# Kernel optimization log

Hardware: AMD Instinct MI355X
Metric: run time of the kernel (lower is better)

## Reference

```python
import jax, jax.numpy as jnp
import numpy as np

NEG_SLOPE = 0.2  # PyG GATConv default


def gat_conv(h, src, dst, n_nodes, W, a_src, a_dst, bias, concat):
    """PyG-style GATConv (single linear shared across src/dst, self-loops
    already included in src/dst). W: [heads*out, in]; a_*: [heads, out]."""
    heads, out = a_src.shape
    g = (h @ W.T).reshape(-1, heads, out)  # [N, H, D]
    # per-node attention logits, then gather scalars per edge (PyG order)
    al_src = jnp.einsum('nhd,hd->nh', g, a_src)  # [N, H]
    al_dst = jnp.einsum('nhd,hd->nh', g, a_dst)
    e = jax.nn.leaky_relu(al_src[src] + al_dst[dst], NEG_SLOPE)  # [E, H]
    # segment softmax over incoming edges of each dst node
    e_max = jax.ops.segment_max(e, dst, num_segments=n_nodes)
    e_exp = jnp.exp(e - e_max[dst])
    denom = jax.ops.segment_sum(e_exp, dst, num_segments=n_nodes)
    alpha = e_exp / denom[dst]  # every node has a self-loop -> denom > 0
    msg = g[src] * alpha[..., None]  # [E, H, D]
    out_n = jax.ops.segment_sum(msg, dst, num_segments=n_nodes)  # [N, H, D]
    if concat:
        out_n = out_n.reshape(n_nodes, heads * out)
    else:
        out_n = out_n.mean(axis=1)
    return out_n + bias


def setup_inputs() -> dict:
    key = jax.random.key(0)
    ks = jax.random.split(key, 20)
    N, M = 100000, 1600000
    node_dim, edge_dim, global_dim = 12, 5, 11
    hidden, heads, num_targets = 32, 4, 4
    in1 = node_dim + global_dim  # 23
    s = 0.1
    inp = {
        'x': jax.random.normal(ks[0], (N, node_dim), jnp.float32),
        'edge_index': jax.random.randint(ks[1], (2, M), 0, N, jnp.int32),
        'edge_attr': jax.random.normal(ks[2], (M, edge_dim), jnp.float32),
        'u': jax.random.normal(ks[3], (1, global_dim), jnp.float32),
        # conv1: in1 -> hidden per head, concat
        'W1': jax.random.normal(ks[4], (heads * hidden, in1), jnp.float32) * s,
        'a_src1': jax.random.normal(ks[5], (heads, hidden), jnp.float32) * s,
        'a_dst1': jax.random.normal(ks[6], (heads, hidden), jnp.float32) * s,
        'b1': jnp.zeros((heads * hidden,), jnp.float32),
        # conv2: heads*hidden -> hidden, mean over heads
        'W2': jax.random.normal(ks[7], (heads * hidden, heads * hidden), jnp.float32) * s,
        'a_src2': jax.random.normal(ks[8], (heads, hidden), jnp.float32) * s,
        'a_dst2': jax.random.normal(ks[9], (heads, hidden), jnp.float32) * s,
        'b2': jnp.zeros((hidden,), jnp.float32),
        # decoder: (2*hidden + edge_dim) -> 2*hidden -> hidden -> num_targets
        'dw1': jax.random.normal(ks[10], (2 * hidden, 2 * hidden + edge_dim), jnp.float32) * s,
        'db1': jnp.zeros((2 * hidden,), jnp.float32),
        'dw2': jax.random.normal(ks[11], (hidden, 2 * hidden), jnp.float32) * s,
        'db2': jnp.zeros((hidden,), jnp.float32),
        'dw3': jax.random.normal(ks[12], (num_targets, hidden), jnp.float32) * s,
        'db3': jnp.zeros((num_targets,), jnp.float32),
    }
    return inp


def reference(x, edge_index, edge_attr, u, W1, a_src1, a_dst1, b1,
              W2, a_src2, a_dst2, b2, dw1, db1, dw2, db2, dw3, db3):
    N = x.shape[0]
    loop = jnp.arange(N, dtype=edge_index.dtype)
    src = jnp.concatenate([edge_index[0], loop])  # add self-loops (PyG default)
    dst = jnp.concatenate([edge_index[1], loop])

    u_node = jnp.broadcast_to(u, (N, u.shape[-1]))
    h = jnp.concatenate([x, u_node], axis=-1)  # [N, 23]

    h = jax.nn.elu(gat_conv(h, src, dst, N, W1, a_src1, a_dst1, b1, True))
    h = jax.nn.elu(gat_conv(h, src, dst, N, W2, a_src2, a_dst2, b2, False))

    s0, d0 = edge_index[0], edge_index[1]
    e_in = jnp.concatenate([h[s0], h[d0], edge_attr], axis=-1)  # [M, 69]
    z = jax.nn.relu(e_in @ dw1.T + db1)
    z = jax.nn.relu(z @ dw2.T + db2)
    return z @ dw3.T + db3  # [M, num_targets]
```

## Files before the change

### kernel.cpp

```cpp
#include <hip/hip_runtime.h>

#define DEVINL __device__ __forceinline__

DEVINL float leakyf(float v) { return v > 0.f ? v : 0.2f * v; }
DEVINL float eluf(float v)   { return v > 0.f ? v : __expf(v) - 1.f; }

__global__ void __launch_bounds__(256) k_izero(int* __restrict__ p, int total) {
  int t = blockIdx.x * blockDim.x + threadIdx.x;
  if (t < total) p[t] = 0;
}

__global__ void __launch_bounds__(256) k_count(const int* __restrict__ ei,
                                               int* __restrict__ cnt, int M, int E) {
  int e = blockIdx.x * blockDim.x + threadIdx.x;
  if (e >= E) return;
  int d = (e < M) ? ei[M + e] : e - M;
  atomicAdd(&cnt[d], 1);
}

__global__ void __launch_bounds__(256) k_scan1(const int* __restrict__ cnt,
                                               int* __restrict__ off,
                                               int* __restrict__ bsum, int N) {
  __shared__ int sh[256];
  int i = blockIdx.x * 256 + threadIdx.x;
  int v = (i < N) ? cnt[i] : 0;
  sh[threadIdx.x] = v;
  __syncthreads();
  for (int o = 1; o < 256; o <<= 1) {
    int t = (threadIdx.x >= o) ? sh[threadIdx.x - o] : 0;
    __syncthreads();
    sh[threadIdx.x] += t;
    __syncthreads();
  }
  if (i < N) off[i] = sh[threadIdx.x] - v;
  if (threadIdx.x == 255) bsum[blockIdx.x] = sh[255];
}

__global__ void __launch_bounds__(512) k_scan2(int* __restrict__ bsum, int nb) {
  __shared__ int sh[512];
  int t = threadIdx.x;
  int v = (t < nb) ? bsum[t] : 0;
  sh[t] = v;
  __syncthreads();
  for (int o = 1; o < 512; o <<= 1) {
    int x = (t >= o) ? sh[t - o] : 0;
    __syncthreads();
    sh[t] += x;
    __syncthreads();
  }
  if (t < nb) bsum[t] = sh[t] - v;
}

__global__ void __launch_bounds__(256) k_scan3(int* __restrict__ off,
                                               const int* __restrict__ bsum,
                                               int* __restrict__ cur, int N, int E) {
  int i = blockIdx.x * 256 + threadIdx.x;
  if (i < N) { off[i] += bsum[i >> 8]; cur[i] = 0; }
  if (i == N) off[N] = E;
}

__global__ void __launch_bounds__(256) k_fill(const int* __restrict__ ei,
                                              const int* __restrict__ off,
                                              int* __restrict__ cur,
                                              int* __restrict__ ssrc, int M, int E) {
  int e = blockIdx.x * blockDim.x + threadIdx.x;
  if (e >= E) return;
  int s, d;
  if (e < M) { s = ei[e]; d = ei[M + e]; } else { s = e - M; d = s; }
  int pos = off[d] + atomicAdd(&cur[d], 1);
  ssrc[pos] = s;
}

__global__ void k_prep(const float* __restrict__ W1, const float* __restrict__ as1,
                       const float* __restrict__ ad1,
                       const float* __restrict__ W2, const float* __restrict__ as2,
                       const float* __restrict__ ad2,
                       float* __restrict__ wa1s, float* __restrict__ wa1d,
                       float* __restrict__ wa2s, float* __restrict__ wa2d) {
  int t = threadIdx.x;
  if (t < 92) {
    int h = t / 23, c = t % 23;
    float s1 = 0.f, s2 = 0.f;
    for (int dd = 0; dd < 32; ++dd) {
      float w = W1[(h * 32 + dd) * 23 + c];
      s1 += w * as1[h * 32 + dd];
      s2 += w * ad1[h * 32 + dd];
    }
    wa1s[t] = s1;
    wa1d[t] = s2;
  }
  {
    int h = t >> 7, c = t & 127;
    float s1 = 0.f, s2 = 0.f;
    for (int dd = 0; dd < 32; ++dd) {
      float w = W2[(h * 32 + dd) * 128 + c];
      s1 += w * as2[h * 32 + dd];
      s2 += w * ad2[h * 32 + dd];
    }
    wa2s[t] = s1;
    wa2d[t] = s2;
  }
}

__global__ void __launch_bounds__(128) k_g1(
    const float* __restrict__ x, const float* __restrict__ u,
    const float* __restrict__ W1,
    const float* __restrict__ wa1s, const float* __restrict__ wa1d,
    float* __restrict__ g1, float* __restrict__ al1s, float* __restrict__ al1d) {
  int n = blockIdx.x, k = threadIdx.x;
  __shared__ float hs[23];
  if (k < 12) hs[k] = x[n * 12 + k];
  else if (k < 23) hs[k] = u[k - 12];
  __syncthreads();
  const float* w = W1 + k * 23;
  float s = 0.f;
#pragma unroll
  for (int c = 0; c < 23; ++c) s += hs[c] * w[c];
  g1[n * 128 + k] = s;
  if (k < 8) {
    int h = k & 3;
    const float* wa = (k < 4 ? wa1s : wa1d) + h * 23;
    float t = 0.f;
#pragma unroll
    for (int c = 0; c < 23; ++c) t += hs[c] * wa[c];
    (k < 4 ? al1s : al1d)[n * 4 + h] = t;
  }
}

template <int MODE>
__global__ void __launch_bounds__(128) k_gat(
    const float* __restrict__ g, const float* __restrict__ als,
    const float* __restrict__ ald, const int* __restrict__ off,
    const int* __restrict__ ssrc, const float* __restrict__ bias,
    float* __restrict__ outp) {
  int d = blockIdx.x, t = threadIdx.x, h = t >> 5;
  float av = ald[d * 4 + h];
  int p0 = off[d], p1 = off[d + 1];
  float acc = 0.f, den = 0.f;
  int sA = ssrc[p0];
  for (int p = p0; p < p1;) {
    int s = sA;
    int pn = p + 1;
    if (pn < p1) sA = ssrc[pn];
    float w = __expf(leakyf(als[s * 4 + h] + av));
    acc += w * g[(size_t)s * 128 + t];
    den += w;
    p = pn;
  }
  float v = acc / den;
  if (MODE == 0) {
    outp[(size_t)d * 128 + t] = eluf(v + bias[t]);
  } else {
    __shared__ float sh[128];
    sh[t] = v;
    __syncthreads();
    if (t < 32) {
      float m = 0.25f * (sh[t] + sh[t + 32] + sh[t + 64] + sh[t + 96]);
      outp[(size_t)d * 32 + t] = eluf(m + bias[t]);
    }
  }
}

__global__ void __launch_bounds__(128) k_g2t(
    const float* __restrict__ h2, const float* __restrict__ W2,
    const float* __restrict__ wa2s, const float* __restrict__ wa2d,
    float* __restrict__ g2, float* __restrict__ al2s, float* __restrict__ al2d,
    int N, int ntiles) {
  __shared__ float4 w4s[128][32];
  __shared__ float4 hs4[32][32];
  int t = threadIdx.x;

  for (int i = t; i < 4096; i += 128) {
    int c = i >> 5, kk = i & 31;
    float4 v = *(const float4*)(W2 + c * 128 + kk * 4);
    w4s[c][kk ^ ((c >> 2) & 31)] = v;
  }

  int m = t & 31, grp = t >> 5;
  int c0 = 4 * m;

  for (int tile = blockIdx.x; tile < ntiles; tile += gridDim.x) {
    int n0 = tile * 32;
    __syncthreads();
    for (int i = t; i < 1024; i += 128) {
      int n = i >> 5, kk = i & 31;
      int nn = n0 + n;
      hs4[n][kk] = (nn < N) ? *(const float4*)(h2 + (size_t)nn * 128 + kk * 4)
                            : make_float4(0.f, 0.f, 0.f, 0.f);
    }
    __syncthreads();

    float acc[8][4];
#pragma unroll
    for (int n = 0; n < 8; ++n)
#pragma unroll
      for (int j = 0; j < 4; ++j) acc[n][j] = 0.f;

#pragma unroll 8
    for (int kk = 0; kk < 32; ++kk) {
      float4 wj[4];
#pragma unroll
      for (int j = 0; j < 4; ++j) wj[j] = w4s[c0 + j][kk ^ m];
#pragma unroll
      for (int n = 0; n < 8; ++n) {
        float4 hv = hs4[grp * 8 + n][kk];
#pragma unroll
        for (int j = 0; j < 4; ++j) {
          acc[n][j] += hv.x * wj[j].x + hv.y * wj[j].y +
                       hv.z * wj[j].z + hv.w * wj[j].w;
        }
      }
    }
#pragma unroll
    for (int n = 0; n < 8; ++n) {
      int nn = n0 + grp * 8 + n;
      if (nn < N)
        *(float4*)(g2 + (size_t)nn * 128 + c0) =
            make_float4(acc[n][0], acc[n][1], acc[n][2], acc[n][3]);
    }

    for (int v = 0; v < 2; ++v) {
      int idx = t + 128 * v;
      int n = idx >> 3, j = idx & 7, h = j & 3;
      int nn = n0 + n;
      if (nn < N) {
        const float4* wa = (const float4*)((j < 4 ? wa2s : wa2d) + h * 128);
        float s = 0.f;
#pragma unroll
        for (int kk = 0; kk < 32; ++kk) {
          float4 a = hs4[n][kk];
          float4 w = wa[kk];
          s += a.x * w.x + a.y * w.y + a.z * w.z + a.w * w.w;
        }
        (j < 4 ? al2s : al2d)[(size_t)nn * 4 + h] = s;
      }
    }
  }
}

__global__ void __launch_bounds__(256) k_pq(
    const float* __restrict__ h3, const float* __restrict__ dw1,
    float* __restrict__ pq, int N) {
  __shared__ float4 ws4[64][16];
  __shared__ float ht[64][32];
  int t = threadIdx.x;
  for (int i = t; i < 4096; i += 256) {
    int k = i >> 6, c = i & 63;
    ((float*)&ws4[k][(c >> 2) ^ (k & 15)])[c & 3] = dw1[k * 69 + c];
  }
  int n0 = blockIdx.x * 64;
  for (int i = t; i < 2048; i += 256) {
    int n = i >> 5, c = i & 31;
    int nn = n0 + n;
    ht[n][c] = (nn < N) ? h3[(size_t)nn * 32 + c] : 0.f;
  }
  __syncthreads();
  int k2 = t & 127, sub = t >> 7;
  int k = k2 & 63, base4 = (k2 < 64) ? 0 : 8;
  float4 wr[8];
#pragma unroll
  for (int i = 0; i < 8; ++i) wr[i] = ws4[k][(base4 + i) ^ (k & 15)];
  for (int ii = 0; ii < 32; ++ii) {
    int n = sub * 32 + ii;
    const float4* hr = (const float4*)ht[n];
    float s = 0.f;
#pragma unroll
    for (int i = 0; i < 8; ++i) {
      float4 a = hr[i], w = wr[i];
      s += a.x * w.x + a.y * w.y + a.z * w.z + a.w * w.w;
    }
    int nn = n0 + n;
    if (nn < N) pq[(size_t)nn * 128 + k2] = s;
  }
}

__global__ void __launch_bounds__(256) k_dec(
    const float* __restrict__ pq, const int* __restrict__ ei,
    const float* __restrict__ ea,
    const float* __restrict__ dw1, const float* __restrict__ db1,
    const float* __restrict__ dw2, const float* __restrict__ db2,
    const float* __restrict__ dw3, const float* __restrict__ db3,
    float* __restrict__ out, int M) {
  __shared__ float cs[64][8];
  __shared__ float w2s[32 * 64];
  __shared__ float w3s[4 * 32];
  __shared__ float bbs[104];
  int t = threadIdx.x;
  for (int i = t; i < 512; i += 256) {
    int k = i >> 3, c = i & 7;
    cs[k][c] = (c < 5) ? dw1[k * 69 + 64 + c] : 0.f;
  }
  for (int i = t; i < 2048; i += 256) w2s[i] = dw2[i];
  if (t < 128) w3s[t] = dw3[t];
  if (t < 64) bbs[t] = db1[t];
  else if (t < 96) bbs[t] = db2[t - 64];
  else if (t < 100) bbs[t] = db3[t - 96];
  __syncthreads();

  int m = blockIdx.x * 256 + t;
  if (m >= M) return;
  int s = ei[m], d = ei[M + m];
  const float4* Pp = (const float4*)(pq + (size_t)s * 128);
  const float4* Qp = (const float4*)(pq + (size_t)d * 128 + 64);
  const float* ep = ea + (size_t)m * 5;
  float e0 = ep[0], e1 = ep[1], e2 = ep[2], e3 = ep[3], e4 = ep[4];

  float z1[64];
#pragma unroll
  for (int i = 0; i < 16; ++i) {
    float4 p = Pp[i], q = Qp[i];
    z1[4 * i + 0] = p.x + q.x;
    z1[4 * i + 1] = p.y + q.y;
    z1[4 * i + 2] = p.z + q.z;
    z1[4 * i + 3] = p.w + q.w;
  }
#pragma unroll
  for (int k = 0; k < 64; ++k) {
    float acc = z1[k] + bbs[k];
    acc += cs[k][0] * e0 + cs[k][1] * e1 + cs[k][2] * e2 + cs[k][3] * e3 +
           cs[k][4] * e4;
    z1[k] = fmaxf(acc, 0.f);
  }

  float z2[32];
#pragma unroll
  for (int k = 0; k < 32; ++k) z2[k] = bbs[64 + k];
#pragma unroll
  for (int cq = 0; cq < 16; ++cq) {
    float4 e = make_float4(z1[cq * 4], z1[cq * 4 + 1], z1[cq * 4 + 2],
                           z1[cq * 4 + 3]);
#pragma unroll
    for (int k = 0; k < 32; ++k) {
      float4 w = *(const float4*)(w2s + k * 64 + cq * 4);
      z2[k] += e.x * w.x + e.y * w.y + e.z * w.z + e.w * w.w;
    }
  }
#pragma unroll
  for (int k = 0; k < 32; ++k) z2[k] = fmaxf(z2[k], 0.f);

  float o0 = bbs[96], o1 = bbs[97], o2 = bbs[98], o3 = bbs[99];
#pragma unroll
  for (int cq = 0; cq < 8; ++cq) {
    float4 e = make_float4(z2[cq * 4], z2[cq * 4 + 1], z2[cq * 4 + 2],
                           z2[cq * 4 + 3]);
    float4 wa = *(const float4*)(w3s + 0 * 32 + cq * 4);
    float4 wb = *(const float4*)(w3s + 1 * 32 + cq * 4);
    float4 wc = *(const float4*)(w3s + 2 * 32 + cq * 4);
    float4 wd = *(const float4*)(w3s + 3 * 32 + cq * 4);
    o0 += e.x * wa.x + e.y * wa.y + e.z * wa.z + e.w * wa.w;
    o1 += e.x * wb.x + e.y * wb.y + e.z * wb.z + e.w * wb.w;
    o2 += e.x * wc.x + e.y * wc.y + e.z * wc.z + e.w * wc.w;
    o3 += e.x * wd.x + e.y * wd.y + e.z * wd.z + e.w * wd.w;
  }
  *(float4*)(out + (size_t)m * 4) = make_float4(o0, o1, o2, o3);
}

extern "C" void kernel_launch(void* const* d_in, const int* in_sizes, int n_in,
                              void* d_out, int out_size, void* d_ws, size_t ws_size,
                              hipStream_t stream) {
  const float* x   = (const float*)d_in[0];
  const int*   ei  = (const int*)d_in[1];
  const float* ea  = (const float*)d_in[2];
  const float* u   = (const float*)d_in[3];
  const float* W1  = (const float*)d_in[4];
  const float* as1 = (const float*)d_in[5];
  const float* ad1 = (const float*)d_in[6];
  const float* b1  = (const float*)d_in[7];
  const float* W2  = (const float*)d_in[8];
  const float* as2 = (const float*)d_in[9];
  const float* ad2 = (const float*)d_in[10];
  const float* b2  = (const float*)d_in[11];
  const float* dw1 = (const float*)d_in[12];
  const float* db1 = (const float*)d_in[13];
  const float* dw2 = (const float*)d_in[14];
  const float* db2 = (const float*)d_in[15];
  const float* dw3 = (const float*)d_in[16];
  const float* db3 = (const float*)d_in[17];
  float* out = (float*)d_out;

  const int N = in_sizes[0] / 12;
  const int M = in_sizes[1] / 2;
  const int E = M + N;

  float* ws = (float*)d_ws;
  float* A    = ws;
  float* B    = A + (size_t)N * 128;
  float* H3   = B + (size_t)N * 128;
  float* AL1S = H3 + (size_t)N * 32;
  float* AL1D = AL1S + (size_t)N * 4;
  float* AL2S = AL1D + (size_t)N * 4;
  float* AL2D = AL2S + (size_t)N * 4;
  float* WA1S = AL2D + (size_t)N * 4;
  float* WA1D = WA1S + 96;
  float* WA2S = WA1D + 96;
  float* WA2D = WA2S + 512;
  int* IOFF = (int*)(WA2D + 512);
  int* ICUR = IOFF + (N + 1);
  int* IBS  = ICUR + N;
  int* ISRC = IBS + 512;

  int nb = (N + 255) / 256;
  int gE = (E + 255) / 256;

  k_izero<<<nb, 256, 0, stream>>>(ICUR, N);
  k_count<<<gE, 256, 0, stream>>>(ei, ICUR, M, E);
  k_scan1<<<nb, 256, 0, stream>>>(ICUR, IOFF, IBS, N);
  k_scan2<<<1, 512, 0, stream>>>(IBS, nb);
  k_scan3<<<(N + 256) / 256, 256, 0, stream>>>(IOFF, IBS, ICUR, N, E);
  k_fill<<<gE, 256, 0, stream>>>(ei, IOFF, ICUR, ISRC, M, E);

  k_prep<<<1, 512, 0, stream>>>(W1, as1, ad1, W2, as2, ad2, WA1S, WA1D, WA2S, WA2D);

  k_g1<<<N, 128, 0, stream>>>(x, u, W1, WA1S, WA1D, A, AL1S, AL1D);
  k_gat<0><<<N, 128, 0, stream>>>(A, AL1S, AL1D, IOFF, ISRC, b1, B);

  int ntiles = (N + 31) / 32;
  k_g2t<<<512, 128, 0, stream>>>(B, W2, WA2S, WA2D, A, AL2S, AL2D, N, ntiles);
  k_gat<1><<<N, 128, 0, stream>>>(A, AL2S, AL2D, IOFF, ISRC, b2, H3);

  k_pq<<<(N + 63) / 64, 256, 0, stream>>>(H3, dw1, A, N);
  k_dec<<<(M + 255) / 256, 256, 0, stream>>>(A, ei, ea, dw1, db1, dw2, db2,
                                             dw3, db3, out, M);
}
```

Before: 1.240 ms.

## Process decoder edges in dst-sorted CSR order and unroll GAT gather loop

The fill kernel now also records destination and original edge id per CSR slot, and the edge decoder walks edges in dst-sorted order. Consecutive threads then share the destination row of pq, which improves cache reuse, while edge_attr reads and output writes become scattered through the edge id and self-loop slots leave idle threads. The GAT aggregation loop is unrolled by four so several independent gathers are in flight at once, and H3 now aliases buffer B to shrink the workspace.

After: 1.122 ms. 1.11x faster.

```diff
diff --git a/kernel.cpp b/kernel.cpp
--- a/kernel.cpp
+++ b/kernel.cpp
@@ -62,13 +62,18 @@
 __global__ void __launch_bounds__(256) k_fill(const int* __restrict__ ei,
                                               const int* __restrict__ off,
                                               int* __restrict__ cur,
-                                              int* __restrict__ ssrc, int M, int E) {
+                                              int* __restrict__ ssrc,
+                                              int* __restrict__ idst,
+                                              int* __restrict__ ieid, int M, int E) {
   int e = blockIdx.x * blockDim.x + threadIdx.x;
   if (e >= E) return;
-  int s, d;
-  if (e < M) { s = ei[e]; d = ei[M + e]; } else { s = e - M; d = s; }
+  int s, d, id;
+  if (e < M) { s = ei[e]; d = ei[M + e]; id = e; }
+  else       { s = e - M; d = s; id = -1; }
   int pos = off[d] + atomicAdd(&cur[d], 1);
   ssrc[pos] = s;
+  idst[pos] = d;
+  ieid[pos] = id;
 }
 
 __global__ void k_prep(const float* __restrict__ W1, const float* __restrict__ as1,
@@ -137,15 +142,23 @@
   float av = ald[d * 4 + h];
   int p0 = off[d], p1 = off[d + 1];
   float acc = 0.f, den = 0.f;
-  int sA = ssrc[p0];
-  for (int p = p0; p < p1;) {
-    int s = sA;
-    int pn = p + 1;
-    if (pn < p1) sA = ssrc[pn];
+  int p = p0;
+  for (; p + 4 <= p1; p += 4) {
+    int s0 = ssrc[p], s1 = ssrc[p + 1], s2 = ssrc[p + 2], s3 = ssrc[p + 3];
+    float l0 = als[s0 * 4 + h], l1 = als[s1 * 4 + h];
+    float l2 = als[s2 * 4 + h], l3 = als[s3 * 4 + h];
+    float g0 = g[(size_t)s0 * 128 + t], g1v = g[(size_t)s1 * 128 + t];
+    float g2v = g[(size_t)s2 * 128 + t], g3v = g[(size_t)s3 * 128 + t];
+    float w0 = __expf(leakyf(l0 + av)), w1 = __expf(leakyf(l1 + av));
+    float w2 = __expf(leakyf(l2 + av)), w3 = __expf(leakyf(l3 + av));
+    acc += w0 * g0 + w1 * g1v + w2 * g2v + w3 * g3v;
+    den += (w0 + w1) + (w2 + w3);
+  }
+  for (; p < p1; ++p) {
+    int s = ssrc[p];
     float w = __expf(leakyf(als[s * 4 + h] + av));
     acc += w * g[(size_t)s * 128 + t];
     den += w;
-    p = pn;
   }
   float v = acc / den;
   if (MODE == 0) {
@@ -275,12 +288,13 @@
 }
 
 __global__ void __launch_bounds__(256) k_dec(
-    const float* __restrict__ pq, const int* __restrict__ ei,
+    const float* __restrict__ pq, const int* __restrict__ ssrc,
+    const int* __restrict__ idst, const int* __restrict__ ieid,
     const float* __restrict__ ea,
     const float* __restrict__ dw1, const float* __restrict__ db1,
     const float* __restrict__ dw2, const float* __restrict__ db2,
     const float* __restrict__ dw3, const float* __restrict__ db3,
-    float* __restrict__ out, int M) {
+    float* __restrict__ out, int E) {
   __shared__ float cs[64][8];
   __shared__ float w2s[32 * 64];
   __shared__ float w3s[4 * 32];
@@ -297,12 +311,14 @@
   else if (t < 100) bbs[t] = db3[t - 96];
   __syncthreads();
 
-  int m = blockIdx.x * 256 + t;
-  if (m >= M) return;
-  int s = ei[m], d = ei[M + m];
+  int pos = blockIdx.x * 256 + t;
+  if (pos >= E) return;
+  int eid = ieid[pos];
+  if (eid < 0) return;
+  int s = ssrc[pos], d = idst[pos];
   const float4* Pp = (const float4*)(pq + (size_t)s * 128);
   const float4* Qp = (const float4*)(pq + (size_t)d * 128 + 64);
-  const float* ep = ea + (size_t)m * 5;
+  const float* ep = ea + (size_t)eid * 5;
   float e0 = ep[0], e1 = ep[1], e2 = ep[2], e3 = ep[3], e4 = ep[4];
 
   float z1[64];
@@ -352,7 +368,7 @@
     o2 += e.x * wc.x + e.y * wc.y + e.z * wc.z + e.w * wc.w;
     o3 += e.x * wd.x + e.y * wd.y + e.z * wd.z + e.w * wd.w;
   }
-  *(float4*)(out + (size_t)m * 4) = make_float4(o0, o1, o2, o3);
+  *(float4*)(out + (size_t)eid * 4) = make_float4(o0, o1, o2, o3);
 }
 
 extern "C" void kernel_launch(void* const* d_in, const int* in_sizes, int n_in,
@@ -385,8 +401,8 @@
   float* ws = (float*)d_ws;
   float* A    = ws;
   float* B    = A + (size_t)N * 128;
-  float* H3   = B + (size_t)N * 128;
-  float* AL1S = H3 + (size_t)N * 32;
+  float* H3   = B;
+  float* AL1S = B + (size_t)N * 128;
   float* AL1D = AL1S + (size_t)N * 4;
   float* AL2S = AL1D + (size_t)N * 4;
   float* AL2D = AL2S + (size_t)N * 4;
@@ -398,6 +414,8 @@
   int* ICUR = IOFF + (N + 1);
   int* IBS  = ICUR + N;
   int* ISRC = IBS + 512;
+  int* IDST = ISRC + E;
+  int* IEID = IDST + E;
 
   int nb = (N + 255) / 256;
   int gE = (E + 255) / 256;
@@ -407,7 +425,7 @@
   k_scan1<<<nb, 256, 0, stream>>>(ICUR, IOFF, IBS, N);
   k_scan2<<<1, 512, 0, stream>>>(IBS, nb);
   k_scan3<<<(N + 256) / 256, 256, 0, stream>>>(IOFF, IBS, ICUR, N, E);
-  k_fill<<<gE, 256, 0, stream>>>(ei, IOFF, ICUR, ISRC, M, E);
+  k_fill<<<gE, 256, 0, stream>>>(ei, IOFF, ICUR, ISRC, IDST, IEID, M, E);
 
   k_prep<<<1, 512, 0, stream>>>(W1, as1, ad1, W2, as2, ad2, WA1S, WA1D, WA2S, WA2D);
 
@@ -419,6 +437,6 @@
   k_gat<1><<<N, 128, 0, stream>>>(A, AL2S, AL2D, IOFF, ISRC, b2, H3);
 
   k_pq<<<(N + 63) / 64, 256, 0, stream>>>(H3, dw1, A, N);
-  k_dec<<<(M + 255) / 256, 256, 0, stream>>>(A, ei, ea, dw1, db1, dw2, db2,
-                                             dw3, db3, out, M);
-}
+  k_dec<<<gE, 256, 0, stream>>>(A, ISRC, IDST, IEID, ea, dw1, db1, dw2, db2,
+                                dw3, db3, out, E);
+}
```
